# Kernel optimization log

Measured on AMD Instinct MI355X. Metric: run time of the kernel, lower is better.

## Reference

```python
import jax, jax.numpy as jnp
import numpy as np

SPARSITY_PROB = 0.1
CAUSAL = True
B, H, S, D = 2, 16, 2048, 64


def _make_mask(key, seq_len, sparsity_prob, causal):
    # random_mask = rand < p, optionally AND causal tril, then force diagonal True
    m = jax.random.uniform(key, (seq_len, seq_len)) < sparsity_prob
    if causal:
        m = m & jnp.tril(jnp.ones((seq_len, seq_len), dtype=bool))
    idx = jnp.arange(seq_len)
    m = m.at[idx, idx].set(True)
    return m


def setup_inputs() -> dict:
    key = jax.random.key(0)
    kq, kk, kv, km = jax.random.split(key, 4)
    query = jax.random.normal(kq, (B, H, S, D), dtype=jnp.float32)
    k_ = jax.random.normal(kk, (B, H, S, D), dtype=jnp.float32)
    v_ = jax.random.normal(kv, (B, H, S, D), dtype=jnp.float32)
    mask = _make_mask(km, S, SPARSITY_PROB, CAUSAL)
    return {"query": query, "key": k_, "value": v_, "mask": mask}


def reference(query, key, value, mask):
    # Masked attention: softmax over the selected positions of each row is
    # mathematically identical to the per-row gather+softmax in the original.
    # mask: [S, S] bool, shared across batch and heads; every row has at least
    # the diagonal True, so no fully-masked rows.
    head_dim = query.shape[-1]
    scale = 1.0 / jnp.sqrt(jnp.asarray(head_dim, dtype=query.dtype))
    scores = jnp.einsum("bhqd,bhkd->bhqk", query, key) * scale  # [B,H,S,S]
    scores = jnp.where(mask[None, None, :, :], scores, -jnp.inf)
    attn = jax.nn.softmax(scores, axis=-1)
    return jnp.einsum("bhqk,bhkd->bhqd", attn, value)
```

## Files before the change

### kernel.cpp

```cpp
#include <hip/hip_runtime.h>
#include <hip/hip_bf16.h>

#define SEQ 2048
#define HD 64
#define NBH 32
#define SCALE 0.125f
#define QSC 0.18033688011112042f

typedef __attribute__((ext_vector_type(4)))  float    f32x4;
typedef __attribute__((ext_vector_type(16))) float    f32x16;
typedef __attribute__((ext_vector_type(8)))  short    bf16x8;
typedef __attribute__((ext_vector_type(4)))  unsigned u32x4;

__device__ inline short f2bf(float f) {
    unsigned u = __builtin_bit_cast(unsigned, f);
    unsigned r = u + 0x7FFFu + ((u >> 16) & 1u);
    return (short)(r >> 16);
}

__device__ inline unsigned cvt2(float lo, float hi) {
    unsigned d;
    asm("v_cvt_pk_bf16_f32 %0, %1, %2" : "=v"(d) : "v"(lo), "v"(hi));
    return d;
}

__global__ void detect_mask_kernel(const unsigned char* __restrict__ m, int n, int* flag) {
    if (threadIdx.x == 0) *flag = (m[n - 1] != 0) ? 1 : 4;
}

__global__ __launch_bounds__(256)
void prep_kernel(const unsigned char* __restrict__ m, const int* __restrict__ flag,
                 const float* __restrict__ K, const float* __restrict__ V,
                 unsigned* __restrict__ bits, short* __restrict__ Kb,
                 short* __restrict__ Vt) {
    __shared__ short t[64][65];
    const int b = blockIdx.x, tid = threadIdx.x;
    if (b < 512) {
        const int idx = b * 256 + tid;
        const int row = idx >> 6, w = idx & 63;
        const size_t base = (size_t)row * SEQ + w * 32;
        unsigned word = 0;
        if (*flag == 1) {
            #pragma unroll
            for (int i = 0; i < 32; ++i) word |= (unsigned)(m[base + i] != 0) << i;
        } else {
            const unsigned* m32 = (const unsigned*)m;
            #pragma unroll
            for (int i = 0; i < 32; ++i) word |= (unsigned)(m32[base + i] != 0) << i;
        }
        bits[(size_t)w * SEQ + row] = word;
    } else if (b < 2560) {
        const int g = (b - 512) * 256 + tid;
        const size_t i = (size_t)g * 8;
        f32x4 a = *(const f32x4*)(K + i);
        f32x4 c = *(const f32x4*)(K + i + 4);
        bf16x8 o;
        #pragma unroll
        for (int j = 0; j < 4; ++j) { o[j] = f2bf(a[j]); o[4 + j] = f2bf(c[j]); }
        const int row = g >> 3;
        const int c8  = g & 7;
        const int bh  = row >> 11;
        const int r   = row & 2047;
        const int tt  = r >> 5;
        const int la  = r & 31;
        *(bf16x8*)(Kb + ((size_t)bh * 64 + tt) * 2048 + (c8 * 32 + la) * 8) = o;
    } else {
        const int bb = b - 2560;
        const int s0 = (bb & 31) * 64, bh = bb >> 5;
        const float* Vb = V + (size_t)bh * SEQ * HD;
        const int sr = tid >> 6, d = tid & 63;
        #pragma unroll
        for (int i = 0; i < 16; ++i) {
            const int s = i * 4 + sr;
            t[s][d] = f2bf(Vb[(size_t)(s0 + s) * HD + d]);
        }
        __syncthreads();
        short* o = Vt + (size_t)bh * HD * SEQ;
        const int dr = tid >> 6, sl = tid & 63;
        #pragma unroll
        for (int i = 0; i < 16; ++i) {
            const int dd = i * 4 + dr;
            const int s = s0 + sl;
            const int k = s & 31;
            const int p = (k & ~12) | ((k & 8) >> 1) | ((k & 4) << 1);
            const int mm = ((dd >> 5) << 1) | (p >> 4);
            const int hh = (p >> 3) & 1;
            o[(size_t)(s >> 5) * 2048 + ((mm * 2 + hh) * 32 + (dd & 31)) * 8 + (p & 7)] = t[sl][dd];
        }
    }
}

__global__ __launch_bounds__(256, 2)
void attn_half_kernel(const float* __restrict__ Q, const short* __restrict__ Kb,
                      const short* __restrict__ Vt, const unsigned* __restrict__ bitsT,
                      short* __restrict__ Oh_ws, float* __restrict__ l_ws) {
    __shared__ __align__(16) short pool[16384];
    short* kpool = pool;
    short* vpool = pool + 8192;

    const int id   = blockIdx.x;
    const int bh   = id & 31;
    const int s8   = (id >> 5) & 7;
    const int g    = id >> 8;
    int qg, half;
    if (g == 0)      { qg = 15 - s8; half = 0; }
    else if (g == 1) { qg = 8 + s8;  half = 1; }
    else if (g == 2) { qg = 7 - s8;  half = 0; }
    else             { qg = s8;      half = 1; }

    const int tid  = threadIdx.x;
    const int wid  = tid >> 6;
    const int lane = tid & 63;
    const int la   = lane & 31;
    const int h    = lane >> 5;
    const int q0w  = qg * 128 + wid * 32;
    const int htiles = 2 * qg + 2;
    const int tstart = half * htiles;
    const int tend   = tstart + htiles;

    bf16x8 qf[4];
    {
        const float* qp = Q + (size_t)bh * SEQ * HD + (size_t)(q0w + la) * HD + h * 8;
        #pragma unroll
        for (int j = 0; j < 4; ++j) {
            f32x4 a0 = *(const f32x4*)(qp + j * 16);
            f32x4 a1 = *(const f32x4*)(qp + j * 16 + 4);
            #pragma unroll
            for (int i = 0; i < 4; ++i) {
                qf[j][i]     = f2bf(a0[i] * QSC);
                qf[j][4 + i] = f2bf(a1[i] * QSC);
            }
        }
    }

    f32x16 acc_o0 = {0,0,0,0,0,0,0,0,0,0,0,0,0,0,0,0};
    f32x16 acc_o1 = {0,0,0,0,0,0,0,0,0,0,0,0,0,0,0,0};
    float l_run = 0.f;

    const short* Ktg = Kb + (size_t)bh * 64 * 2048;
    const short* Vtg = Vt + (size_t)bh * 64 * 2048;
    const unsigned* bq = bitsT + q0w + la;
    const int bp = 4 * h;

    auto body = [&](const short* kb, const short* vb, unsigned mwx) {
        bf16x8 kfa = *(const bf16x8*)(kb + lane * 8);
        bf16x8 kfb = *(const bf16x8*)(kb + 512 + lane * 8);
        bf16x8 kfc = *(const bf16x8*)(kb + 1024 + lane * 8);
        bf16x8 kfd = *(const bf16x8*)(kb + 1536 + lane * 8);
        bf16x8 vf00 = *(const bf16x8*)(vb + lane * 8);
        bf16x8 vf01 = *(const bf16x8*)(vb + 512 + lane * 8);
        bf16x8 vf10 = *(const bf16x8*)(vb + 1024 + lane * 8);
        bf16x8 vf11 = *(const bf16x8*)(vb + 1536 + lane * 8);

        f32x16 sA = {0,0,0,0,0,0,0,0,0,0,0,0,0,0,0,0};
        f32x16 sB = {0,0,0,0,0,0,0,0,0,0,0,0,0,0,0,0};
        __builtin_amdgcn_s_setprio(1);
        sA = __builtin_amdgcn_mfma_f32_32x32x16_bf16(kfa, qf[0], sA, 0, 0, 0);
        sB = __builtin_amdgcn_mfma_f32_32x32x16_bf16(kfc, qf[2], sB, 0, 0, 0);
        sA = __builtin_amdgcn_mfma_f32_32x32x16_bf16(kfb, qf[1], sA, 0, 0, 0);
        sB = __builtin_amdgcn_mfma_f32_32x32x16_bf16(kfd, qf[3], sB, 0, 0, 0);
        __builtin_amdgcn_s_setprio(0);
        f32x16 s = sA + sB;

        #pragma unroll
        for (int r = 0; r < 16; ++r) {
            float e = __builtin_amdgcn_exp2f(s[r]);
            s[r] = ((mwx >> (bp + (r & 3) + 8 * (r >> 2))) & 1u) ? e : 0.f;
        }
        float ps = ((s[0] + s[1]) + (s[2] + s[3])) + ((s[4] + s[5]) + (s[6] + s[7]));
        ps += ((s[8] + s[9]) + (s[10] + s[11])) + ((s[12] + s[13]) + (s[14] + s[15]));
        l_run += ps;

        u32x4 t1 = {cvt2(s[0], s[1]),  cvt2(s[2], s[3]),
                    cvt2(s[4], s[5]),  cvt2(s[6], s[7])};
        u32x4 t2 = {cvt2(s[8], s[9]),  cvt2(s[10], s[11]),
                    cvt2(s[12], s[13]), cvt2(s[14], s[15])};
        bf16x8 pb1 = __builtin_bit_cast(bf16x8, t1);
        bf16x8 pb2 = __builtin_bit_cast(bf16x8, t2);

        __builtin_amdgcn_s_setprio(1);
        acc_o0 = __builtin_amdgcn_mfma_f32_32x32x16_bf16(vf00, pb1, acc_o0, 0, 0, 0);
        acc_o1 = __builtin_amdgcn_mfma_f32_32x32x16_bf16(vf10, pb1, acc_o1, 0, 0, 0);
        acc_o0 = __builtin_amdgcn_mfma_f32_32x32x16_bf16(vf01, pb2, acc_o0, 0, 0, 0);
        acc_o1 = __builtin_amdgcn_mfma_f32_32x32x16_bf16(vf11, pb2, acc_o1, 0, 0, 0);
        __builtin_amdgcn_s_setprio(0);
    };

    {
        bf16x8 k0 = *(const bf16x8*)(Ktg + (size_t)tstart * 2048 + tid * 8);
        bf16x8 k1 = *(const bf16x8*)(Ktg + (size_t)(tstart + 1) * 2048 + tid * 8);
        bf16x8 v0 = *(const bf16x8*)(Vtg + (size_t)tstart * 2048 + tid * 8);
        bf16x8 v1 = *(const bf16x8*)(Vtg + (size_t)(tstart + 1) * 2048 + tid * 8);
        *(bf16x8*)(kpool + tid * 8) = k0;
        *(bf16x8*)(kpool + 2048 + tid * 8) = k1;
        *(bf16x8*)(vpool + tid * 8) = v0;
        *(bf16x8*)(vpool + 2048 + tid * 8) = v1;
    }
    unsigned mw0 = bq[(size_t)tstart * SEQ];
    unsigned mw1 = bq[(size_t)(tstart + 1) * SEQ];

    int cur = 0;
    for (int t = tstart; t < tend; t += 2) {
        __syncthreads();

        int tn0 = t + 2, tn1 = t + 3;
        if (t + 2 >= tend) { tn0 = t; tn1 = t + 1; }
        bf16x8 sk0 = *(const bf16x8*)(Ktg + (size_t)tn0 * 2048 + tid * 8);
        bf16x8 sk1 = *(const bf16x8*)(Ktg + (size_t)tn1 * 2048 + tid * 8);
        bf16x8 sv0 = *(const bf16x8*)(Vtg + (size_t)tn0 * 2048 + tid * 8);
        bf16x8 sv1 = *(const bf16x8*)(Vtg + (size_t)tn1 * 2048 + tid * 8);
        unsigned nmw0 = bq[(size_t)tn0 * SEQ];
        unsigned nmw1 = bq[(size_t)tn1 * SEQ];

        body(kpool + cur * 4096, vpool + cur * 4096, mw0);
        body(kpool + cur * 4096 + 2048, vpool + cur * 4096 + 2048, mw1);

        *(bf16x8*)(kpool + (cur ^ 1) * 4096 + tid * 8) = sk0;
        *(bf16x8*)(kpool + (cur ^ 1) * 4096 + 2048 + tid * 8) = sk1;
        *(bf16x8*)(vpool + (cur ^ 1) * 4096 + tid * 8) = sv0;
        *(bf16x8*)(vpool + (cur ^ 1) * 4096 + 2048 + tid * 8) = sv1;

        mw0 = nmw0; mw1 = nmw1;
        cur ^= 1;
    }

    const int slot = (qg * 32 + bh) * 2 + half;

    const float l_full = l_run + __shfl_xor(l_run, 32);
    const float invw = (l_full > 0.f) ? (1.f / l_full) : 0.f;
    if (h == 0) l_ws[(size_t)slot * 128 + wid * 32 + la] = l_full;

    __syncthreads();

    short (*oacc)[32][72] = (short (*)[32][72])pool;
    {
        unsigned short* orow = (unsigned short*)&oacc[wid][la][0];
        #pragma unroll
        for (int g2 = 0; g2 < 4; ++g2) {
            const int d0 = 8 * g2 + 4 * h;
            unsigned w0 = cvt2(acc_o0[4 * g2 + 0] * invw, acc_o0[4 * g2 + 1] * invw);
            unsigned w1 = cvt2(acc_o0[4 * g2 + 2] * invw, acc_o0[4 * g2 + 3] * invw);
            unsigned w2 = cvt2(acc_o1[4 * g2 + 0] * invw, acc_o1[4 * g2 + 1] * invw);
            unsigned w3 = cvt2(acc_o1[4 * g2 + 2] * invw, acc_o1[4 * g2 + 3] * invw);
            *(unsigned*)&orow[d0]      = w0;
            *(unsigned*)&orow[d0 + 2]  = w1;
            *(unsigned*)&orow[d0 + 32] = w2;
            *(unsigned*)&orow[d0 + 34] = w3;
        }
    }
    __syncthreads();

    {
        const int q  = tid >> 3;
        const int dc = (tid & 7) * 8;
        unsigned short* ob = (unsigned short*)Oh_ws + (size_t)slot * 8192;
        #pragma unroll
        for (int k = 0; k < 4; ++k) {
            u32x4 pk = *(const u32x4*)&oacc[k][q][dc];
            *(u32x4*)(ob + (k * 32 + q) * 64 + dc) = pk;
        }
    }
}

__global__ __launch_bounds__(256)
void reduce_kernel(const short* __restrict__ Oh_ws, const float* __restrict__ l_ws,
                   float* __restrict__ Out) {
    const int id = blockIdx.x;
    const int group = id >> 2;
    const int sub = id & 3;
    const int qg = group >> 5, bh = group & 31;
    const int tid = threadIdx.x;
    const int q  = sub * 32 + (tid >> 3);
    const int dc = (tid & 7) * 8;
    const size_t s0 = (size_t)(group * 2);

    const float l0 = l_ws[s0 * 128 + q];
    const float l1 = l_ws[(s0 + 1) * 128 + q];
    const float inv = 1.f / (l0 + l1);
    u32x4 p0 = *(const u32x4*)((const unsigned short*)Oh_ws + s0 * 8192 + q * 64 + dc);
    u32x4 p1 = *(const u32x4*)((const unsigned short*)Oh_ws + (s0 + 1) * 8192 + q * 64 + dc);
    float o[8];
    #pragma unroll
    for (int j = 0; j < 4; ++j) {
        float a0 = __builtin_bit_cast(float, (p0[j] & 0xFFFFu) << 16);
        float a1 = __builtin_bit_cast(float, p0[j] & 0xFFFF0000u);
        float b0 = __builtin_bit_cast(float, (p1[j] & 0xFFFFu) << 16);
        float b1 = __builtin_bit_cast(float, p1[j] & 0xFFFF0000u);
        o[2 * j]     = (l0 * a0 + l1 * b0) * inv;
        o[2 * j + 1] = (l0 * a1 + l1 * b1) * inv;
    }
    float* op = Out + (size_t)bh * SEQ * HD + (size_t)(qg * 128 + q) * HD + dc;
    f32x4 o0v = {o[0], o[1], o[2], o[3]};
    f32x4 o1v = {o[4], o[5], o[6], o[7]};
    *(f32x4*)op       = o0v;
    *(f32x4*)(op + 4) = o1v;
}

__global__ __launch_bounds__(256, 2)
void attn_shared_kernel(const float* __restrict__ Q, const short* __restrict__ Kb,
                        const short* __restrict__ Vt, const unsigned* __restrict__ bitsT,
                        float* __restrict__ Out) {
    __shared__ __align__(16) short kbuf[2][2][2048];
    __shared__ __align__(16) short vbuf[2][2][2048];
    __shared__ short oacc[4][32][72];

    const int id   = blockIdx.x;
    const int bh   = id & 31;
    const int qg   = (id < 256) ? (15 - (id >> 5)) : ((id - 256) >> 5);
    const int tid  = threadIdx.x;
    const int wid  = tid >> 6;
    const int lane = tid & 63;
    const int la   = lane & 31;
    const int h    = lane >> 5;
    const int q0w  = qg * 128 + wid * 32;
    const int nt   = qg * 4 + 4;
    const size_t base = (size_t)bh * SEQ * HD;

    bf16x8 qf[4];
    {
        const float* qp = Q + base + (size_t)(q0w + la) * HD + h * 8;
        #pragma unroll
        for (int j = 0; j < 4; ++j) {
            f32x4 a0 = *(const f32x4*)(qp + j * 16);
            f32x4 a1 = *(const f32x4*)(qp + j * 16 + 4);
            #pragma unroll
            for (int i = 0; i < 4; ++i) {
                qf[j][i]     = f2bf(a0[i] * QSC);
                qf[j][4 + i] = f2bf(a1[i] * QSC);
            }
        }
    }

    f32x16 acc_o0 = {0,0,0,0,0,0,0,0,0,0,0,0,0,0,0,0};
    f32x16 acc_o1 = {0,0,0,0,0,0,0,0,0,0,0,0,0,0,0,0};
    float l_run = 0.f;

    const short* Ktg = Kb + (size_t)bh * 64 * 2048;
    const short* Vtg = Vt + (size_t)bh * 64 * 2048;
    const unsigned* bq = bitsT + q0w + la;
    const int bp = 4 * h;

    auto body = [&](const short* kb, const short* vb, unsigned mwx) {
        bf16x8 kfa = *(const bf16x8*)(kb + lane * 8);
        bf16x8 kfb = *(const bf16x8*)(kb + 512 + lane * 8);
        bf16x8 kfc = *(const bf16x8*)(kb + 1024 + lane * 8);
        bf16x8 kfd = *(const bf16x8*)(kb + 1536 + lane * 8);
        bf16x8 vf00 = *(const bf16x8*)(vb + lane * 8);
        bf16x8 vf01 = *(const bf16x8*)(vb + 512 + lane * 8);
        bf16x8 vf10 = *(const bf16x8*)(vb + 1024 + lane * 8);
        bf16x8 vf11 = *(const bf16x8*)(vb + 1536 + lane * 8);

        f32x16 sA = {0,0,0,0,0,0,0,0,0,0,0,0,0,0,0,0};
        f32x16 sB = {0,0,0,0,0,0,0,0,0,0,0,0,0,0,0,0};
        __builtin_amdgcn_s_setprio(1);
        sA = __builtin_amdgcn_mfma_f32_32x32x16_bf16(kfa, qf[0], sA, 0, 0, 0);
        sB = __builtin_amdgcn_mfma_f32_32x32x16_bf16(kfc, qf[2], sB, 0, 0, 0);
        sA = __builtin_amdgcn_mfma_f32_32x32x16_bf16(kfb, qf[1], sA, 0, 0, 0);
        sB = __builtin_amdgcn_mfma_f32_32x32x16_bf16(kfd, qf[3], sB, 0, 0, 0);
        __builtin_amdgcn_s_setprio(0);
        f32x16 s = sA + sB;

        #pragma unroll
        for (int r = 0; r < 16; ++r) {
            float e = __builtin_amdgcn_exp2f(s[r]);
            s[r] = ((mwx >> (bp + (r & 3) + 8 * (r >> 2))) & 1u) ? e : 0.f;
        }
        float ps = ((s[0] + s[1]) + (s[2] + s[3])) + ((s[4] + s[5]) + (s[6] + s[7]));
        ps += ((s[8] + s[9]) + (s[10] + s[11])) + ((s[12] + s[13]) + (s[14] + s[15]));
        l_run += ps;

        u32x4 t1 = {cvt2(s[0], s[1]),  cvt2(s[2], s[3]),
                    cvt2(s[4], s[5]),  cvt2(s[6], s[7])};
        u32x4 t2 = {cvt2(s[8], s[9]),  cvt2(s[10], s[11]),
                    cvt2(s[12], s[13]), cvt2(s[14], s[15])};
        bf16x8 pb1 = __builtin_bit_cast(bf16x8, t1);
        bf16x8 pb2 = __builtin_bit_cast(bf16x8, t2);

        __builtin_amdgcn_s_setprio(1);
        acc_o0 = __builtin_amdgcn_mfma_f32_32x32x16_bf16(vf00, pb1, acc_o0, 0, 0, 0);
        acc_o1 = __builtin_amdgcn_mfma_f32_32x32x16_bf16(vf10, pb1, acc_o1, 0, 0, 0);
        acc_o0 = __builtin_amdgcn_mfma_f32_32x32x16_bf16(vf01, pb2, acc_o0, 0, 0, 0);
        acc_o1 = __builtin_amdgcn_mfma_f32_32x32x16_bf16(vf11, pb2, acc_o1, 0, 0, 0);
        __builtin_amdgcn_s_setprio(0);
    };

    {
        bf16x8 k0 = *(const bf16x8*)(Ktg + (size_t)tid * 8);
        bf16x8 k1 = *(const bf16x8*)(Ktg + 2048 + (size_t)tid * 8);
        bf16x8 v0 = *(const bf16x8*)(Vtg + (size_t)tid * 8);
        bf16x8 v1 = *(const bf16x8*)(Vtg + 2048 + (size_t)tid * 8);
        *(bf16x8*)(&kbuf[0][0][0] + tid * 8) = k0;
        *(bf16x8*)(&kbuf[0][1][0] + tid * 8) = k1;
        *(bf16x8*)(&vbuf[0][0][0] + tid * 8) = v0;
        *(bf16x8*)(&vbuf[0][1][0] + tid * 8) = v1;
    }
    unsigned mw0 = bq[0];
    unsigned mw1 = bq[SEQ];

    int cur = 0;
    for (int t = 0; t < nt; t += 2) {
        __syncthreads();
        const int tn0 = (t + 2 < nt) ? t + 2 : t;
        const int tn1 = (t + 3 < nt) ? t + 3 : t;
        bf16x8 sk0 = *(const bf16x8*)(Ktg + (size_t)tn0 * 2048 + tid * 8);
        bf16x8 sk1 = *(const bf16x8*)(Ktg + (size_t)tn1 * 2048 + tid * 8);
        bf16x8 sv0 = *(const bf16x8*)(Vtg + (size_t)tn0 * 2048 + tid * 8);
        bf16x8 sv1 = *(const bf16x8*)(Vtg + (size_t)tn1 * 2048 + tid * 8);
        unsigned nmw0 = bq[(size_t)tn0 * SEQ];
        unsigned nmw1 = bq[(size_t)tn1 * SEQ];

        body(&kbuf[cur][0][0], &vbuf[cur][0][0], mw0);
        body(&kbuf[cur][1][0], &vbuf[cur][1][0], mw1);

        *(bf16x8*)(&kbuf[cur ^ 1][0][0] + tid * 8) = sk0;
        *(bf16x8*)(&kbuf[cur ^ 1][1][0] + tid * 8) = sk1;
        *(bf16x8*)(&vbuf[cur ^ 1][0][0] + tid * 8) = sv0;
        *(bf16x8*)(&vbuf[cur ^ 1][1][0] + tid * 8) = sv1;

        mw0 = nmw0; mw1 = nmw1;
        cur ^= 1;
    }

    {
        const float l_full = l_run + __shfl_xor(l_run, 32);
        const float invw = 1.f / l_full;
        unsigned short* orow = (unsigned short*)&oacc[wid][la][0];
        #pragma unroll
        for (int g = 0; g < 4; ++g) {
            const int d0 = 8 * g + 4 * h;
            unsigned w0 = cvt2(acc_o0[4 * g + 0] * invw, acc_o0[4 * g + 1] * invw);
            unsigned w1 = cvt2(acc_o0[4 * g + 2] * invw, acc_o0[4 * g + 3] * invw);
            unsigned w2 = cvt2(acc_o1[4 * g + 0] * invw, acc_o1[4 * g + 1] * invw);
            unsigned w3 = cvt2(acc_o1[4 * g + 2] * invw, acc_o1[4 * g + 3] * invw);
            *(unsigned*)&orow[d0]      = w0;
            *(unsigned*)&orow[d0 + 2]  = w1;
            *(unsigned*)&orow[d0 + 32] = w2;
            *(unsigned*)&orow[d0 + 34] = w3;
        }
    }
    __syncthreads();

    {
        const int q  = tid >> 3;
        const int dc = (tid & 7) * 8;
        #pragma unroll
        for (int k = 0; k < 4; ++k) {
            u32x4 pk = *(const u32x4*)&oacc[k][q][dc];
            float o[8];
            #pragma unroll
            for (int j = 0; j < 4; ++j) {
                o[2 * j]     = __builtin_bit_cast(float, (pk[j] & 0xFFFFu) << 16);
                o[2 * j + 1] = __builtin_bit_cast(float, pk[j] & 0xFFFF0000u);
            }
            float* op = Out + base + (size_t)(qg * 128 + k * 32 + q) * HD + dc;
            f32x4 o0v = {o[0], o[1], o[2], o[3]};
            f32x4 o1v = {o[4], o[5], o[6], o[7]};
            *(f32x4*)op       = o0v;
            *(f32x4*)(op + 4) = o1v;
        }
    }
}

__global__ __launch_bounds__(256)
void attn_kernel(const float* __restrict__ Q, const float* __restrict__ K,
                 const float* __restrict__ V, const unsigned char* __restrict__ mask,
                 const int* __restrict__ flag, float* __restrict__ Out) {
    __shared__ short plds[4][16][40];
    const int esz  = *flag;
    const int bh   = blockIdx.y;
    const int wid  = threadIdx.x >> 6;
    const int lane = threadIdx.x & 63;
    const int l16  = lane & 15;
    const int hi   = lane >> 4;
    const int q0   = blockIdx.x * 64 + wid * 16;
    const size_t base = (size_t)bh * SEQ * HD;
    const float* Qb = Q + base;
    const float* Kb = K + base;
    const float* Vb = V + base;
    const unsigned int* mask32 = (const unsigned int*)mask;
    bf16x8 qf[2];
    {
        const float* qp = Qb + (size_t)(q0 + l16) * HD + hi * 8;
        f32x4 a0 = *(const f32x4*)(qp);
        f32x4 a1 = *(const f32x4*)(qp + 4);
        f32x4 a2 = *(const f32x4*)(qp + 32);
        f32x4 a3 = *(const f32x4*)(qp + 36);
        #pragma unroll
        for (int i = 0; i < 4; ++i) {
            qf[0][i] = f2bf(a0[i]); qf[0][4 + i] = f2bf(a1[i]);
            qf[1][i] = f2bf(a2[i]); qf[1][4 + i] = f2bf(a3[i]);
        }
    }
    f32x4 acc_o[4] = {f32x4{0,0,0,0}, f32x4{0,0,0,0}, f32x4{0,0,0,0}, f32x4{0,0,0,0}};
    float m_run[4], l_run[4];
    #pragma unroll
    for (int j = 0; j < 4; ++j) { m_run[j] = -__builtin_inff(); l_run[j] = 0.f; }
    const int kv_end = q0 + 16;
    for (int kv = 0; kv < kv_end; kv += 32) {
        f32x4 acc_s[2] = {f32x4{0,0,0,0}, f32x4{0,0,0,0}};
        #pragma unroll
        for (int t = 0; t < 2; ++t) {
            const float* kp = Kb + (size_t)(kv + 16 * t + l16) * HD + hi * 8;
            f32x4 b0 = *(const f32x4*)(kp);
            f32x4 b1 = *(const f32x4*)(kp + 4);
            f32x4 b2 = *(const f32x4*)(kp + 32);
            f32x4 b3 = *(const f32x4*)(kp + 36);
            bf16x8 kf0, kf1;
            #pragma unroll
            for (int i = 0; i < 4; ++i) {
                kf0[i] = f2bf(b0[i]); kf0[4 + i] = f2bf(b1[i]);
                kf1[i] = f2bf(b2[i]); kf1[4 + i] = f2bf(b3[i]);
            }
            acc_s[t] = __builtin_amdgcn_mfma_f32_16x16x32_bf16(qf[0], kf0, acc_s[t], 0, 0, 0);
            acc_s[t] = __builtin_amdgcn_mfma_f32_16x16x32_bf16(qf[1], kf1, acc_s[t], 0, 0, 0);
        }
        float s[2][4];
        #pragma unroll
        for (int t = 0; t < 2; ++t) {
            const int k = kv + 16 * t + l16;
            #pragma unroll
            for (int j = 0; j < 4; ++j) {
                const int qrow = q0 + hi * 4 + j;
                const size_t midx = (size_t)qrow * SEQ + k;
                const bool mv = (esz == 1) ? (mask[midx] != 0) : (mask32[midx] != 0);
                s[t][j] = mv ? acc_s[t][j] * SCALE : -__builtin_inff();
            }
        }
        float mnew[4], r[4];
        #pragma unroll
        for (int j = 0; j < 4; ++j) {
            float v = fmaxf(s[0][j], s[1][j]);
            #pragma unroll
            for (int off = 1; off < 16; off <<= 1) v = fmaxf(v, __shfl_xor(v, off));
            mnew[j] = fmaxf(m_run[j], v);
            r[j] = (m_run[j] > -__builtin_inff()) ? __expf(m_run[j] - mnew[j]) : 0.f;
        }
        float p[2][4];
        #pragma unroll
        for (int j = 0; j < 4; ++j) {
            float ps = 0.f;
            #pragma unroll
            for (int t = 0; t < 2; ++t) {
                p[t][j] = (s[t][j] > -__builtin_inff()) ? __expf(s[t][j] - mnew[j]) : 0.f;
                ps += p[t][j];
            }
            #pragma unroll
            for (int off = 1; off < 16; off <<= 1) ps += __shfl_xor(ps, off);
            l_run[j] = l_run[j] * r[j] + ps;
            m_run[j] = mnew[j];
            #pragma unroll
            for (int t2 = 0; t2 < 4; ++t2) acc_o[t2][j] *= r[j];
        }
        #pragma unroll
        for (int t = 0; t < 2; ++t)
            #pragma unroll
            for (int j = 0; j < 4; ++j)
                plds[wid][hi * 4 + j][16 * t + l16] = f2bf(p[t][j]);
        bf16x8 pa = *(bf16x8*)&plds[wid][l16][hi * 8];
        #pragma unroll
        for (int t2 = 0; t2 < 4; ++t2) {
            const float* vp = Vb + (size_t)(kv + hi * 8) * HD + 16 * t2 + l16;
            bf16x8 vf;
            #pragma unroll
            for (int i = 0; i < 8; ++i) vf[i] = f2bf(vp[(size_t)i * HD]);
            acc_o[t2] = __builtin_amdgcn_mfma_f32_16x16x32_bf16(pa, vf, acc_o[t2], 0, 0, 0);
        }
    }
    #pragma unroll
    for (int j = 0; j < 4; ++j) {
        const float inv = 1.f / l_run[j];
        const int qrow = q0 + hi * 4 + j;
        float* op = Out + base + (size_t)qrow * HD + l16;
        #pragma unroll
        for (int t2 = 0; t2 < 4; ++t2) op[16 * t2] = acc_o[t2][j] * inv;
    }
}

extern "C" void kernel_launch(void* const* d_in, const int* in_sizes, int n_in,
                              void* d_out, int out_size, void* d_ws, size_t ws_size,
                              hipStream_t stream) {
    const float* Q = (const float*)d_in[0];
    const float* K = (const float*)d_in[1];
    const float* V = (const float*)d_in[2];
    const unsigned char* mask = (const unsigned char*)d_in[3];

    const size_t bitsB = (size_t)SEQ * (SEQ / 32) * 4;
    const size_t kvB   = (size_t)NBH * SEQ * HD * 2;
    const size_t flagB = 256;
    const size_t ohB   = (size_t)1024 * 8192 * 2;
    const size_t lB    = (size_t)1024 * 128 * 4;
    const size_t need_mono  = bitsB + 2 * kvB + flagB;
    const size_t need_split = need_mono + ohB + lB;

    if (ws_size >= need_mono) {
        unsigned* bits = (unsigned*)d_ws;
        short* Kb = (short*)((char*)d_ws + bitsB);
        short* Vt = (short*)((char*)d_ws + bitsB + kvB);
        int* flag = (int*)((char*)d_ws + bitsB + 2 * kvB);

        detect_mask_kernel<<<dim3(1), dim3(64), 0, stream>>>(mask, in_sizes[3], flag);
        prep_kernel<<<dim3(3584), dim3(256), 0, stream>>>(mask, flag, K, V, bits, Kb, Vt);

        if (ws_size >= need_split) {
            short* Oh_ws = (short*)((char*)d_ws + need_mono);
            float* l_ws  = (float*)((char*)d_ws + need_mono + ohB);
            attn_half_kernel<<<dim3(1024), dim3(256), 0, stream>>>(Q, Kb, Vt, bits, Oh_ws, l_ws);
            reduce_kernel<<<dim3(2048), dim3(256), 0, stream>>>(Oh_ws, l_ws, (float*)d_out);
        } else {
            attn_shared_kernel<<<dim3(512), dim3(256), 0, stream>>>(Q, Kb, Vt, bits, (float*)d_out);
        }
    } else {
        int* flag = (int*)d_ws;
        detect_mask_kernel<<<dim3(1), dim3(64), 0, stream>>>(mask, in_sizes[3], flag);
        attn_kernel<<<dim3(SEQ / 64, NBH), dim3(256), 0, stream>>>(Q, K, V, mask, flag, (float*)d_out);
    }
}
```

Baseline: 64.99 us.

## Split causal KV range into fixed 16-tile chunks and drop mask-detect kernel

Replaces the two-halves split-K scheme with fixed-size chunks of 16 KV tiles, so later query groups get up to 4 chunks and early ones get 1. This gives 1280 equal-sized work items instead of 1024 items whose length varies with the query group, which should reduce load imbalance. The reduce kernel now combines a variable number of partials per row. The separate detect_mask launch is also removed, with the mask-format check folded into prep_kernel. In exchange, workspace use grows and the reduce step reads more bf16 partials.

```diff
diff --git a/kernel.cpp b/kernel.cpp
--- a/kernel.cpp
+++ b/kernel.cpp
@@ -29,18 +29,19 @@
 }
 
 __global__ __launch_bounds__(256)
-void prep_kernel(const unsigned char* __restrict__ m, const int* __restrict__ flag,
+void prep_kernel(const unsigned char* __restrict__ m, int mn,
                  const float* __restrict__ K, const float* __restrict__ V,
                  unsigned* __restrict__ bits, short* __restrict__ Kb,
                  short* __restrict__ Vt) {
     __shared__ short t[64][65];
     const int b = blockIdx.x, tid = threadIdx.x;
     if (b < 512) {
+        const bool e1 = (m[mn - 1] != 0);
         const int idx = b * 256 + tid;
         const int row = idx >> 6, w = idx & 63;
         const size_t base = (size_t)row * SEQ + w * 32;
         unsigned word = 0;
-        if (*flag == 1) {
+        if (e1) {
             #pragma unroll
             for (int i = 0; i < 32; ++i) word |= (unsigned)(m[base + i] != 0) << i;
         } else {
@@ -91,22 +92,21 @@
 }
 
 __global__ __launch_bounds__(256, 2)
-void attn_half_kernel(const float* __restrict__ Q, const short* __restrict__ Kb,
-                      const short* __restrict__ Vt, const unsigned* __restrict__ bitsT,
-                      short* __restrict__ Oh_ws, float* __restrict__ l_ws) {
+void attn_chunk_kernel(const float* __restrict__ Q, const short* __restrict__ Kb,
+                       const short* __restrict__ Vt, const unsigned* __restrict__ bitsT,
+                       short* __restrict__ Oh_ws, float* __restrict__ l_ws) {
     __shared__ __align__(16) short pool[16384];
     short* kpool = pool;
     short* vpool = pool + 8192;
 
-    const int id   = blockIdx.x;
-    const int bh   = id & 31;
-    const int s8   = (id >> 5) & 7;
-    const int g    = id >> 8;
-    int qg, half;
-    if (g == 0)      { qg = 15 - s8; half = 0; }
-    else if (g == 1) { qg = 8 + s8;  half = 1; }
-    else if (g == 2) { qg = 7 - s8;  half = 0; }
-    else             { qg = s8;      half = 1; }
+    const int id = blockIdx.x;
+    const int bh = id & 31;
+    const int u  = id >> 5;
+    int qg, c;
+    if (u < 16)      { qg = 12 + (u >> 2);                c = u & 3; }
+    else if (u < 28) { const int v = u - 16; qg = 8 + v / 3; c = v % 3; }
+    else if (u < 36) { const int v = u - 28; qg = 4 + (v >> 1); c = v & 1; }
+    else             { qg = u - 36;                        c = 0; }
 
     const int tid  = threadIdx.x;
     const int wid  = tid >> 6;
@@ -114,9 +114,8 @@
     const int la   = lane & 31;
     const int h    = lane >> 5;
     const int q0w  = qg * 128 + wid * 32;
-    const int htiles = 2 * qg + 2;
-    const int tstart = half * htiles;
-    const int tend   = tstart + htiles;
+    const int tstart = c * 16;
+    const int tend   = min(tstart + 16, 4 * qg + 4);
 
     bf16x8 qf[4];
     {
@@ -224,7 +223,7 @@
         cur ^= 1;
     }
 
-    const int slot = (qg * 32 + bh) * 2 + half;
+    const int slot = u * 32 + bh;
 
     const float l_full = l_run + __shfl_xor(l_run, 32);
     const float invw = (l_full > 0.f) ? (1.f / l_full) : 0.f;
@@ -272,26 +271,32 @@
     const int tid = threadIdx.x;
     const int q  = sub * 32 + (tid >> 3);
     const int dc = (tid & 7) * 8;
-    const size_t s0 = (size_t)(group * 2);
-
-    const float l0 = l_ws[s0 * 128 + q];
-    const float l1 = l_ws[(s0 + 1) * 128 + q];
-    const float inv = 1.f / (l0 + l1);
-    u32x4 p0 = *(const u32x4*)((const unsigned short*)Oh_ws + s0 * 8192 + q * 64 + dc);
-    u32x4 p1 = *(const u32x4*)((const unsigned short*)Oh_ws + (s0 + 1) * 8192 + q * 64 + dc);
-    float o[8];
-    #pragma unroll
-    for (int j = 0; j < 4; ++j) {
-        float a0 = __builtin_bit_cast(float, (p0[j] & 0xFFFFu) << 16);
-        float a1 = __builtin_bit_cast(float, p0[j] & 0xFFFF0000u);
-        float b0 = __builtin_bit_cast(float, (p1[j] & 0xFFFFu) << 16);
-        float b1 = __builtin_bit_cast(float, p1[j] & 0xFFFF0000u);
-        o[2 * j]     = (l0 * a0 + l1 * b0) * inv;
-        o[2 * j + 1] = (l0 * a1 + l1 * b1) * inv;
-    }
+
+    int u0, nch;
+    if (qg >= 12)     { u0 = (qg - 12) * 4;      nch = 4; }
+    else if (qg >= 8) { u0 = 16 + (qg - 8) * 3;  nch = 3; }
+    else if (qg >= 4) { u0 = 28 + (qg - 4) * 2;  nch = 2; }
+    else              { u0 = 36 + qg;            nch = 1; }
+
+    float Lq = 0.f;
+    float o[8] = {0, 0, 0, 0, 0, 0, 0, 0};
+    for (int cc = 0; cc < nch; ++cc) {
+        const size_t slot = (size_t)(u0 + cc) * 32 + bh;
+        const float wl = l_ws[slot * 128 + q];
+        Lq += wl;
+        u32x4 pk = *(const u32x4*)((const unsigned short*)Oh_ws + slot * 8192 + q * 64 + dc);
+        #pragma unroll
+        for (int j = 0; j < 4; ++j) {
+            float lo = __builtin_bit_cast(float, (pk[j] & 0xFFFFu) << 16);
+            float hi = __builtin_bit_cast(float, pk[j] & 0xFFFF0000u);
+            o[2 * j]     += wl * lo;
+            o[2 * j + 1] += wl * hi;
+        }
+    }
+    const float inv = 1.f / Lq;
     float* op = Out + (size_t)bh * SEQ * HD + (size_t)(qg * 128 + q) * HD + dc;
-    f32x4 o0v = {o[0], o[1], o[2], o[3]};
-    f32x4 o1v = {o[4], o[5], o[6], o[7]};
+    f32x4 o0v = {o[0] * inv, o[1] * inv, o[2] * inv, o[3] * inv};
+    f32x4 o1v = {o[4] * inv, o[5] * inv, o[6] * inv, o[7] * inv};
     *(f32x4*)op       = o0v;
     *(f32x4*)(op + 4) = o1v;
 }
@@ -587,24 +592,22 @@
     const size_t bitsB = (size_t)SEQ * (SEQ / 32) * 4;
     const size_t kvB   = (size_t)NBH * SEQ * HD * 2;
     const size_t flagB = 256;
-    const size_t ohB   = (size_t)1024 * 8192 * 2;
-    const size_t lB    = (size_t)1024 * 128 * 4;
+    const size_t ohB   = (size_t)1280 * 8192 * 2;
+    const size_t lB    = (size_t)1280 * 128 * 4;
     const size_t need_mono  = bitsB + 2 * kvB + flagB;
-    const size_t need_split = need_mono + ohB + lB;
+    const size_t need_chunk = need_mono + ohB + lB;
 
     if (ws_size >= need_mono) {
         unsigned* bits = (unsigned*)d_ws;
         short* Kb = (short*)((char*)d_ws + bitsB);
         short* Vt = (short*)((char*)d_ws + bitsB + kvB);
-        int* flag = (int*)((char*)d_ws + bitsB + 2 * kvB);
-
-        detect_mask_kernel<<<dim3(1), dim3(64), 0, stream>>>(mask, in_sizes[3], flag);
-        prep_kernel<<<dim3(3584), dim3(256), 0, stream>>>(mask, flag, K, V, bits, Kb, Vt);
-
-        if (ws_size >= need_split) {
+
+        prep_kernel<<<dim3(3584), dim3(256), 0, stream>>>(mask, in_sizes[3], K, V, bits, Kb, Vt);
+
+        if (ws_size >= need_chunk) {
             short* Oh_ws = (short*)((char*)d_ws + need_mono);
             float* l_ws  = (float*)((char*)d_ws + need_mono + ohB);
-            attn_half_kernel<<<dim3(1024), dim3(256), 0, stream>>>(Q, Kb, Vt, bits, Oh_ws, l_ws);
+            attn_chunk_kernel<<<dim3(1280), dim3(256), 0, stream>>>(Q, Kb, Vt, bits, Oh_ws, l_ws);
             reduce_kernel<<<dim3(2048), dim3(256), 0, stream>>>(Oh_ws, l_ws, (float*)d_out);
         } else {
             attn_shared_kernel<<<dim3(512), dim3(256), 0, stream>>>(Q, Kb, Vt, bits, (float*)d_out);
```

Result: faster. 62.66 us (-3.6%).
